# Kernel optimization log

Hardware: AMD Instinct MI355X
Metric: run time of the kernel (lower is better)

Reference implementation:

```python
import jax, jax.numpy as jnp
import numpy as np

B, N, C, HEADS = 4, 8192, 512, 8


def setup_inputs() -> dict:
    key = jax.random.key(0)
    k1, k2, k3, k4, k5 = jax.random.split(key, 5)
    s = 1.0 / np.sqrt(C)
    return {
        "x": jax.random.normal(k1, (B, N, C), dtype=jnp.float32),
        "w_qkv": jax.random.normal(k2, (3 * C, C), dtype=jnp.float32) * s,
        "b_qkv": jax.random.normal(k3, (3 * C,), dtype=jnp.float32) * 0.01,
        "w_fc": jax.random.normal(k4, (C, C), dtype=jnp.float32) * s,
        "b_fc": jax.random.normal(k5, (C,), dtype=jnp.float32) * 0.01,
        "heads": HEADS,
    }


def reference(x, w_qkv, b_qkv, w_fc, b_fc, heads):
    b, n, c = x.shape
    d = c // heads
    scale = d ** (-0.5)
    # torch Linear: y = x @ W.T + b
    qkv = (x @ w_qkv.T + b_qkv).reshape(b, n, 3, heads, d)
    q, k, v = qkv[:, :, 0], qkv[:, :, 1], qkv[:, :, 2]  # [b,n,h,d]
    # NOTE: source does NOT move heads to dim 1, so attention is over the
    # heads axis: dots is [b, n, h, h].
    dots = jnp.einsum("bnhd,bngd->bnhg", q, k) * scale
    dots = jnp.clip(dots, -50.0, 50.0)
    attn = jax.nn.softmax(dots, axis=-1)
    out = jnp.einsum("bnhg,bngd->bnhd", attn, v)  # [b,n,h,d]
    # transpose(1,2).reshape(B,N,C) exactly as in torch (scrambles n/h)
    out = out.transpose(0, 2, 1, 3).reshape(b, n, c)
    return out @ w_fc.T + b_fc
```

## Files before the change

### kernel.cpp

```cpp
#include <hip/hip_runtime.h>
#include <hip/hip_bf16.h>
#include <stdint.h>


typedef __bf16 bf16x8 __attribute__((ext_vector_type(8)));
typedef float f32x4 __attribute__((ext_vector_type(4)));

__device__ __forceinline__ unsigned short f2bf(float f) {
  unsigned u = __float_as_uint(f);
  u += 0x7fffu + ((u >> 16) & 1u);
  return (unsigned short)(u >> 16);
}
__device__ __forceinline__ unsigned pk2(float a, float b) {
  return (unsigned)f2bf(a) | ((unsigned)f2bf(b) << 16);
}
__device__ __forceinline__ void unpk2(unsigned u, float& a, float& b) {
  a = __uint_as_float(u << 16);
  b = __uint_as_float(u & 0xffff0000u);
}
__device__ __forceinline__ void gload_lds16(const void* g, void* l) {
  __builtin_amdgcn_global_load_lds((const __attribute__((address_space(1))) void*)g,
                                   (__attribute__((address_space(3))) void*)l,
                                   16, 0, 0);
}

__global__ __launch_bounds__(256) void cvt_f32_to_bf16(const float* __restrict__ in,
                                                       __hip_bfloat16* __restrict__ out,
                                                       int n8) {
  int i = blockIdx.x * 256 + threadIdx.x;
  if (i >= n8) return;
  const float4* p = (const float4*)in;
  float4 a = p[i * 2];
  float4 b = p[i * 2 + 1];
  uint4 o;
  o.x = pk2(a.x, a.y);
  o.y = pk2(a.z, a.w);
  o.z = pk2(b.x, b.y);
  o.w = pk2(b.z, b.w);
  ((uint4*)out)[i] = o;
}


#define STG(S, BUF)                                                                       \
  do {                                                                                    \
    int _k0 = (S) * 32;                                                                   \
    gload_lds16(Ag + (size_t)(bm0 + srowA0) * K + _k0 + skofA0,                           \
                lds + (BUF) * 24576 + dstA0);                                             \
    gload_lds16(Ag + (size_t)(bm0 + srowA1) * K + _k0 + skofA1,                           \
                lds + (BUF) * 24576 + dstA1);                                             \
    gload_lds16(Bg + (size_t)(bn0 + srowB) * K + _k0 + skofB,                             \
                lds + (BUF) * 24576 + 16384 + dstB);                                      \
  } while (0)

template <bool OUT_BF16>
__global__ __launch_bounds__(512, 4) void gemm2p(const __hip_bfloat16* __restrict__ Ag,
                                                 const __hip_bfloat16* __restrict__ Bg,
                                                 const float* __restrict__ bias,
                                                 void* __restrict__ C,
                                                 int M, int N, int K, int NT) {
  __shared__ __align__(16) char lds[65536];

  const int tid = threadIdx.x;
  const int wv = tid >> 6;
  const int ln = tid & 63;
  const int lrow = ln & 15;
  const int kg = ln >> 4;
  const int wm = wv >> 1;
  const int wn = wv & 1;

  int nwg = gridDim.x;
  int cpx = nwg >> 3;
  int bs = (blockIdx.x & 7) * cpx + (blockIdx.x >> 3);
  const int bm0 = (bs / NT) * 256;
  const int bn0 = (bs % NT) * 128;

  const int pbase = (lrow >> 1) * 128 + ((((lrow & 1) << 2) | kg) ^ ((lrow >> 1) & 7)) * 16;

  int srowA0, skofA0, dstA0, srowA1, skofA1, dstA1, srowB, skofB, dstB;
  {
    int L0 = wv * 1024 + ln * 16;
    int rp0 = L0 >> 7, T0 = ((L0 >> 4) & 7) ^ (rp0 & 7);
    srowA0 = rp0 * 2 + (T0 >> 2);
    skofA0 = (T0 & 3) * 8;
    dstA0 = wv * 1024;
    int L1 = 8192 + L0;
    int rp1 = L1 >> 7, T1 = ((L1 >> 4) & 7) ^ (rp1 & 7);
    srowA1 = rp1 * 2 + (T1 >> 2);
    skofA1 = (T1 & 3) * 8;
    dstA1 = 8192 + wv * 1024;
    srowB = srowA0;
    skofB = skofA0;
    dstB = wv * 1024;
  }

  f32x4 acc[4][4] = {};

  const int NKT = K >> 5;

  STG(0, 0);
  asm volatile("s_waitcnt vmcnt(0)" ::: "memory");
  __builtin_amdgcn_s_barrier();
  __builtin_amdgcn_sched_barrier(0);

  for (int s = 0; s < NKT; ++s) {
    int b = s & 1;
    if (s + 1 < NKT) STG(s + 1, b ^ 1);
    {
      const char* _ab = lds + b * 24576 + wm * 4096 + pbase;
      const char* _bb = lds + b * 24576 + 16384 + wn * 4096 + pbase;
      bf16x8 a0 = *(const bf16x8*)(_ab);
      bf16x8 a1 = *(const bf16x8*)(_ab + 1024);
      bf16x8 a2 = *(const bf16x8*)(_ab + 2048);
      bf16x8 a3 = *(const bf16x8*)(_ab + 3072);
      bf16x8 b0 = *(const bf16x8*)(_bb);
      bf16x8 b1 = *(const bf16x8*)(_bb + 1024);
      bf16x8 b2 = *(const bf16x8*)(_bb + 2048);
      bf16x8 b3 = *(const bf16x8*)(_bb + 3072);
      asm volatile("s_waitcnt lgkmcnt(0)" ::: "memory");
      __builtin_amdgcn_sched_barrier(0);
      __builtin_amdgcn_s_setprio(1);
      acc[0][0] = __builtin_amdgcn_mfma_f32_16x16x32_bf16(a0, b0, acc[0][0], 0, 0, 0);
      acc[0][1] = __builtin_amdgcn_mfma_f32_16x16x32_bf16(a0, b1, acc[0][1], 0, 0, 0);
      acc[0][2] = __builtin_amdgcn_mfma_f32_16x16x32_bf16(a0, b2, acc[0][2], 0, 0, 0);
      acc[0][3] = __builtin_amdgcn_mfma_f32_16x16x32_bf16(a0, b3, acc[0][3], 0, 0, 0);
      acc[1][0] = __builtin_amdgcn_mfma_f32_16x16x32_bf16(a1, b0, acc[1][0], 0, 0, 0);
      acc[1][1] = __builtin_amdgcn_mfma_f32_16x16x32_bf16(a1, b1, acc[1][1], 0, 0, 0);
      acc[1][2] = __builtin_amdgcn_mfma_f32_16x16x32_bf16(a1, b2, acc[1][2], 0, 0, 0);
      acc[1][3] = __builtin_amdgcn_mfma_f32_16x16x32_bf16(a1, b3, acc[1][3], 0, 0, 0);
      acc[2][0] = __builtin_amdgcn_mfma_f32_16x16x32_bf16(a2, b0, acc[2][0], 0, 0, 0);
      acc[2][1] = __builtin_amdgcn_mfma_f32_16x16x32_bf16(a2, b1, acc[2][1], 0, 0, 0);
      acc[2][2] = __builtin_amdgcn_mfma_f32_16x16x32_bf16(a2, b2, acc[2][2], 0, 0, 0);
      acc[2][3] = __builtin_amdgcn_mfma_f32_16x16x32_bf16(a2, b3, acc[2][3], 0, 0, 0);
      acc[3][0] = __builtin_amdgcn_mfma_f32_16x16x32_bf16(a3, b0, acc[3][0], 0, 0, 0);
      acc[3][1] = __builtin_amdgcn_mfma_f32_16x16x32_bf16(a3, b1, acc[3][1], 0, 0, 0);
      acc[3][2] = __builtin_amdgcn_mfma_f32_16x16x32_bf16(a3, b2, acc[3][2], 0, 0, 0);
      acc[3][3] = __builtin_amdgcn_mfma_f32_16x16x32_bf16(a3, b3, acc[3][3], 0, 0, 0);
      __builtin_amdgcn_s_setprio(0);
    }
    asm volatile("s_waitcnt vmcnt(0)" ::: "memory");
    __builtin_amdgcn_s_barrier();
    __builtin_amdgcn_sched_barrier(0);
  }

  if (OUT_BF16) {
    unsigned short* tile = (unsigned short*)lds;
#pragma unroll
    for (int fi = 0; fi < 4; ++fi) {
#pragma unroll
      for (int cj = 0; cj < 4; ++cj) {
        int col = wn * 64 + cj * 16 + lrow;
        float bv = bias[bn0 + col];
#pragma unroll
        for (int r = 0; r < 4; ++r) {
          int row = wm * 64 + fi * 16 + kg * 4 + r;
          int sc = (((col >> 3) ^ (row & 7)) << 3) | (col & 7);
          tile[row * 128 + sc] = f2bf(acc[fi][cj][r] + bv);
        }
      }
    }
    __syncthreads();
#pragma unroll
    for (int it = 0; it < 8; ++it) {
      int id = it * 512 + tid;
      int row = id >> 4;
      int c = id & 15;
      uint4 v = *(const uint4*)(lds + row * 256 + ((c ^ (row & 7)) << 4));
      *(uint4*)((unsigned short*)C + (size_t)(bm0 + row) * N + bn0 + c * 8) = v;
    }
  } else {
    float* tilef = (float*)lds;
#pragma unroll
    for (int pass = 0; pass < 2; ++pass) {
      if ((wm >> 1) == pass) {
#pragma unroll
        for (int fi = 0; fi < 4; ++fi) {
#pragma unroll
          for (int cj = 0; cj < 4; ++cj) {
            int col = wn * 64 + cj * 16 + lrow;
            float bv = bias[bn0 + col];
#pragma unroll
            for (int r = 0; r < 4; ++r) {
              int row = (wm & 1) * 64 + fi * 16 + kg * 4 + r;
              int sc = (((col >> 2) ^ (row & 7)) << 2) | (col & 3);
              tilef[row * 128 + sc] = acc[fi][cj][r] + bv;
            }
          }
        }
      }
      __syncthreads();
#pragma unroll
      for (int it = 0; it < 8; ++it) {
        int id = it * 512 + tid;
        int row = id >> 5;
        int c = id & 31;
        uint4 v = *(const uint4*)(lds + row * 512 + ((c ^ (row & 7)) << 4));
        *(uint4*)((float*)C + (size_t)(bm0 + pass * 128 + row) * N + bn0 + c * 4) = v;
      }
      __syncthreads();
    }
  }
}

__global__ __launch_bounds__(256) void attn_tok(const __hip_bfloat16* __restrict__ qkv,
                                                __hip_bfloat16* __restrict__ outp,
                                                int ntok, int npb) {
  const int wv = threadIdx.x >> 6;
  const int ln = threadIdx.x & 63;
  const int t = blockIdx.x * 4 + wv;
  if (t >= ntok) return;
  const int m = ln & 7;

  const __hip_bfloat16* row = qkv + (size_t)t * 1536;
  uint4 qr = *(const uint4*)(row + ln * 8);
  uint4 kr = *(const uint4*)(row + 512 + ln * 8);
  uint4 vr = *(const uint4*)(row + 1024 + ln * 8);

  float qf[8];
  unpk2(qr.x, qf[0], qf[1]);
  unpk2(qr.y, qf[2], qf[3]);
  unpk2(qr.z, qf[4], qf[5]);
  unpk2(qr.w, qf[6], qf[7]);
  unsigned kw[4] = {kr.x, kr.y, kr.z, kr.w};
  unsigned vw[4] = {vr.x, vr.y, vr.z, vr.w};

  float dt[8];
#pragma unroll
  for (int g = 0; g < 8; ++g) {
    int src = g * 8 + m;
    float s = 0.f;
#pragma unroll
    for (int j4 = 0; j4 < 4; ++j4) {
      unsigned kk = __shfl(kw[j4], src, 64);
      float a, b;
      unpk2(kk, a, b);
      s += qf[j4 * 2] * a + qf[j4 * 2 + 1] * b;
    }
    s += __shfl_xor(s, 1, 64);
    s += __shfl_xor(s, 2, 64);
    s += __shfl_xor(s, 4, 64);
    dt[g] = s;
  }

  float mx = -1e30f;
#pragma unroll
  for (int g = 0; g < 8; ++g) {
    dt[g] = fminf(fmaxf(dt[g] * 0.125f, -50.f), 50.f);
    mx = fmaxf(mx, dt[g]);
  }
  float p[8], ssum = 0.f;
#pragma unroll
  for (int g = 0; g < 8; ++g) {
    p[g] = __expf(dt[g] - mx);
    ssum += p[g];
  }
  float inv = 1.f / ssum;

  float o[8] = {0, 0, 0, 0, 0, 0, 0, 0};
#pragma unroll
  for (int g = 0; g < 8; ++g) {
    int src = g * 8 + m;
    float ag = p[g] * inv;
#pragma unroll
    for (int j4 = 0; j4 < 4; ++j4) {
      unsigned vv = __shfl(vw[j4], src, 64);
      float a, b;
      unpk2(vv, a, b);
      o[j4 * 2] += ag * a;
      o[j4 * 2 + 1] += ag * b;
    }
  }

  const int h = ln >> 3;
  const int b = t / npb, n = t % npb;
  size_t dst = (size_t)b * npb * 512 + (size_t)(h * (npb >> 3) + (n >> 3)) * 512 +
               (size_t)((n & 7) * 64 + m * 8);
  uint4 ov;
  ov.x = pk2(o[0], o[1]);
  ov.y = pk2(o[2], o[3]);
  ov.z = pk2(o[4], o[5]);
  ov.w = pk2(o[6], o[7]);
  *(uint4*)(outp + dst) = ov;
}

extern "C" void kernel_launch(void* const* d_in, const int* in_sizes, int n_in,
                              void* d_out, int out_size, void* d_ws, size_t ws_size,
                              hipStream_t stream) {
  const float* x = (const float*)d_in[0];
  const float* w_qkv = (const float*)d_in[1];
  const float* b_qkv = (const float*)d_in[2];
  const float* w_fc = (const float*)d_in[3];
  const float* b_fc = (const float*)d_in[4];
  float* out = (float*)d_out;

  const int M = 32768;
  const int Cc = 512, N3 = 1536;

  __hip_bfloat16* xb = (__hip_bfloat16*)d_ws;
  __hip_bfloat16* wqkvb = xb + (size_t)M * Cc;
  __hip_bfloat16* wfcb = wqkvb + (size_t)N3 * Cc;
  __hip_bfloat16* qkvb = wfcb + (size_t)Cc * Cc;
  __hip_bfloat16* attb = qkvb + (size_t)M * N3;

  cvt_f32_to_bf16<<<(M * Cc / 8) / 256, 256, 0, stream>>>(x, xb, M * Cc / 8);
  cvt_f32_to_bf16<<<(N3 * Cc / 8) / 256, 256, 0, stream>>>(w_qkv, wqkvb, N3 * Cc / 8);
  cvt_f32_to_bf16<<<(Cc * Cc / 8) / 256, 256, 0, stream>>>(w_fc, wfcb, Cc * Cc / 8);

  gemm2p<true><<<(M / 256) * (N3 / 128), 512, 0, stream>>>(xb, wqkvb, b_qkv, qkvb, M, N3, Cc,
                                                           N3 / 128);
  attn_tok<<<M / 4, 256, 0, stream>>>(qkvb, attb, M, 8192);
  gemm2p<false><<<(M / 256) * (Cc / 128), 512, 0, stream>>>(attb, wfcb, b_fc, out, M, Cc, Cc,
                                                            Cc / 128);
}
```

Before: 152.4 us.

## Triple-buffer GEMM LDS staging with compile-time K and one barrier per step

Converts the bf16 GEMM from double to triple buffering in LDS, prefetching two K-steps ahead and waiting with a partial vmcnt so loads for the next tiles stay in flight during the MFMA work. K becomes a template constant so the K loop fully unrolls and the buffer indices are resolved at compile time. The cost is a larger LDS footprint (72KB), which may cut how many workgroups fit per CU, and more live state from the unrolled loop.

```diff
diff --git a/kernel.cpp b/kernel.cpp
--- a/kernel.cpp
+++ b/kernel.cpp
@@ -44,21 +44,21 @@
 #define STG(S, BUF)                                                                       \
   do {                                                                                    \
     int _k0 = (S) * 32;                                                                   \
-    gload_lds16(Ag + (size_t)(bm0 + srowA0) * K + _k0 + skofA0,                           \
+    gload_lds16(Ag + (size_t)(bm0 + srowA0) * KDIM + _k0 + skofA0,                        \
                 lds + (BUF) * 24576 + dstA0);                                             \
-    gload_lds16(Ag + (size_t)(bm0 + srowA1) * K + _k0 + skofA1,                           \
+    gload_lds16(Ag + (size_t)(bm0 + srowA1) * KDIM + _k0 + skofA1,                        \
                 lds + (BUF) * 24576 + dstA1);                                             \
-    gload_lds16(Bg + (size_t)(bn0 + srowB) * K + _k0 + skofB,                             \
+    gload_lds16(Bg + (size_t)(bn0 + srowB) * KDIM + _k0 + skofB,                          \
                 lds + (BUF) * 24576 + 16384 + dstB);                                      \
   } while (0)
 
-template <bool OUT_BF16>
-__global__ __launch_bounds__(512, 4) void gemm2p(const __hip_bfloat16* __restrict__ Ag,
+template <bool OUT_BF16, int KDIM>
+__global__ __launch_bounds__(512, 4) void gemm3b(const __hip_bfloat16* __restrict__ Ag,
                                                  const __hip_bfloat16* __restrict__ Bg,
                                                  const float* __restrict__ bias,
                                                  void* __restrict__ C,
-                                                 int M, int N, int K, int NT) {
-  __shared__ __align__(16) char lds[65536];
+                                                 int M, int N, int NT) {
+  __shared__ __align__(16) char lds[73728];
 
   const int tid = threadIdx.x;
   const int wv = tid >> 6;
@@ -95,19 +95,24 @@
 
   f32x4 acc[4][4] = {};
 
-  const int NKT = K >> 5;
+  constexpr int NKT = KDIM >> 5;
 
   STG(0, 0);
-  asm volatile("s_waitcnt vmcnt(0)" ::: "memory");
-  __builtin_amdgcn_s_barrier();
-  __builtin_amdgcn_sched_barrier(0);
-
+  STG(1, 1);
+
+#pragma unroll
   for (int s = 0; s < NKT; ++s) {
-    int b = s & 1;
-    if (s + 1 < NKT) STG(s + 1, b ^ 1);
+    if (s == NKT - 1) {
+      asm volatile("s_waitcnt vmcnt(0)" ::: "memory");
+    } else {
+      asm volatile("s_waitcnt vmcnt(3)" ::: "memory");
+    }
+    __builtin_amdgcn_s_barrier();
+    __builtin_amdgcn_sched_barrier(0);
+    if (s + 2 < NKT) STG(s + 2, (s + 2) % 3);
     {
-      const char* _ab = lds + b * 24576 + wm * 4096 + pbase;
-      const char* _bb = lds + b * 24576 + 16384 + wn * 4096 + pbase;
+      const char* _ab = lds + (s % 3) * 24576 + wm * 4096 + pbase;
+      const char* _bb = lds + (s % 3) * 24576 + 16384 + wn * 4096 + pbase;
       bf16x8 a0 = *(const bf16x8*)(_ab);
       bf16x8 a1 = *(const bf16x8*)(_ab + 1024);
       bf16x8 a2 = *(const bf16x8*)(_ab + 2048);
@@ -137,10 +142,8 @@
       acc[3][3] = __builtin_amdgcn_mfma_f32_16x16x32_bf16(a3, b3, acc[3][3], 0, 0, 0);
       __builtin_amdgcn_s_setprio(0);
     }
-    asm volatile("s_waitcnt vmcnt(0)" ::: "memory");
-    __builtin_amdgcn_s_barrier();
-    __builtin_amdgcn_sched_barrier(0);
-  }
+  }
+  __syncthreads();
 
   if (OUT_BF16) {
     unsigned short* tile = (unsigned short*)lds;
@@ -305,9 +308,9 @@
   cvt_f32_to_bf16<<<(N3 * Cc / 8) / 256, 256, 0, stream>>>(w_qkv, wqkvb, N3 * Cc / 8);
   cvt_f32_to_bf16<<<(Cc * Cc / 8) / 256, 256, 0, stream>>>(w_fc, wfcb, Cc * Cc / 8);
 
-  gemm2p<true><<<(M / 256) * (N3 / 128), 512, 0, stream>>>(xb, wqkvb, b_qkv, qkvb, M, N3, Cc,
-                                                           N3 / 128);
+  gemm3b<true, 512><<<(M / 256) * (N3 / 128), 512, 0, stream>>>(xb, wqkvb, b_qkv, qkvb, M, N3,
+                                                                N3 / 128);
   attn_tok<<<M / 4, 256, 0, stream>>>(qkvb, attb, M, 8192);
-  gemm2p<false><<<(M / 256) * (Cc / 128), 512, 0, stream>>>(attb, wfcb, b_fc, out, M, Cc, Cc,
-                                                            Cc / 128);
-}
+  gemm3b<false, 512><<<(M / 256) * (Cc / 128), 512, 0, stream>>>(attb, wfcb, b_fc, out, M, Cc,
+                                                                 Cc / 128);
+}
```

New measurement: 147.4 us. -3.3%, faster.
